# Kernel tuning notes

Hardware: AMD Instinct MI355X
Metric: run time of the kernel (lower is better)

The kernel has to match this reference:

```python
import jax, jax.numpy as jnp
import numpy as np

V, C = 100000, 400000          # variables, clauses
IN, OUT, H = 96, 64, 4         # in_channels, out_channels, heads
E_HALF = 1000000               # edges per direction
NEG_SLOPE = 0.2
LN_EPS = 1e-5


def _w(k, shape, fan_in):
    return (jax.random.normal(k, shape, jnp.float32) / np.sqrt(fan_in)).astype(jnp.float32)


def setup_inputs() -> dict:
    key = jax.random.key(0)
    ks = jax.random.split(key, 30)
    x = jax.random.normal(ks[0], (V + C, IN), jnp.float32)
    node_type = jnp.concatenate([jnp.full((V,), 1.0, jnp.float32), jnp.full((C,), 2.0, jnp.float32)])
    x = x.at[:, 0].set(node_type)  # NODE_TYPE_VAR=1, NODE_TYPE_CLAUSE=2
    # first half: "v2c" edges (source id >= num_vars), second half: "c2v" edges
    src1 = jax.random.randint(ks[1], (E_HALF,), V, 2 * V)   # -V -> index into x_var
    dst1 = jax.random.randint(ks[2], (E_HALF,), 0, C)       # index into x_clause
    src2 = jax.random.randint(ks[3], (E_HALF,), 0, V)       # index into h_c_new (V<=C so valid)
    dst2 = jax.random.randint(ks[4], (E_HALF,), V, 2 * V)   # -V -> index into x_var
    edge_index = jnp.stack([jnp.concatenate([src1, src2]),
                            jnp.concatenate([dst1, dst2])]).astype(jnp.int32)
    HD = H * OUT
    return {
        "x": x, "edge_index": edge_index, "num_vars": V,
        # v2c GATv2Conv (src=vars IN, dst=clauses IN)
        "v2c_Wl": _w(ks[5], (IN, HD), IN), "v2c_Wr": _w(ks[6], (IN, HD), IN),
        "v2c_att": _w(ks[7], (H, OUT), OUT), "v2c_bias": jnp.zeros((HD,), jnp.float32),
        "c_ln_g": jnp.ones((HD,), jnp.float32), "c_ln_b": jnp.zeros((HD,), jnp.float32),
        "c_Wih": _w(ks[8], (3 * OUT, HD), HD), "c_Whh": _w(ks[9], (3 * OUT, OUT), OUT),
        "c_bih": jnp.zeros((3 * OUT,), jnp.float32), "c_bhh": jnp.zeros((3 * OUT,), jnp.float32),
        # c2v GATv2Conv (src=clauses OUT, dst=vars IN)
        "c2v_Wl": _w(ks[10], (OUT, HD), OUT), "c2v_Wr": _w(ks[11], (IN, HD), IN),
        "c2v_att": _w(ks[12], (H, OUT), OUT), "c2v_bias": jnp.zeros((HD,), jnp.float32),
        "v_ln_g": jnp.ones((HD,), jnp.float32), "v_ln_b": jnp.zeros((HD,), jnp.float32),
        "v_Wih": _w(ks[13], (3 * OUT, HD), HD), "v_Whh": _w(ks[14], (3 * OUT, OUT), OUT),
        "v_bih": jnp.zeros((3 * OUT,), jnp.float32), "v_bhh": jnp.zeros((3 * OUT,), jnp.float32),
    }


def gatv2(x_src, x_dst, edge_index, Wl, Wr, att, bias, num_dst):
    """PyG GATv2Conv, concat=True, no self loops, eval mode (no attn dropout)."""
    h, d = att.shape
    xl = (x_src @ Wl).reshape(-1, h, d)   # [Ns, H, D]
    xr = (x_dst @ Wr).reshape(-1, h, d)   # [Nd, H, D]
    j, i = edge_index[0], edge_index[1]
    e = jax.nn.leaky_relu(xl[j] + xr[i], NEG_SLOPE)          # [E, H, D]
    alpha = jnp.einsum('ehd,hd->eh', e, att)                 # [E, H]
    amax = jax.ops.segment_max(alpha, i, num_segments=num_dst)
    alpha = jnp.exp(alpha - amax[i])
    denom = jax.ops.segment_sum(alpha, i, num_segments=num_dst)
    alpha = alpha / (denom[i] + 1e-16)
    msg = xl[j] * alpha[..., None]                           # [E, H, D]
    out = jax.ops.segment_sum(msg, i, num_segments=num_dst)  # [num_dst, H, D]
    return out.reshape(num_dst, h * d) + bias


def layernorm(x, g, b):
    mu = jnp.mean(x, axis=-1, keepdims=True)
    var = jnp.mean((x - mu) ** 2, axis=-1, keepdims=True)
    return (x - mu) * jax.lax.rsqrt(var + LN_EPS) * g + b


def gru_cell(x, hprev, Wih, Whh, bih, bhh):
    gi = x @ Wih.T + bih      # [N, 3*OUT]
    gh = hprev @ Whh.T + bhh  # [N, 3*OUT]
    ir, iz, inn = jnp.split(gi, 3, axis=-1)
    hr, hz, hn = jnp.split(gh, 3, axis=-1)
    r = jax.nn.sigmoid(ir + hr)
    z = jax.nn.sigmoid(iz + hz)
    n = jnp.tanh(inn + r * hn)
    return (1.0 - z) * n + z * hprev


def reference(x, edge_index, num_vars,
              v2c_Wl, v2c_Wr, v2c_att, v2c_bias, c_ln_g, c_ln_b,
              c_Wih, c_Whh, c_bih, c_bhh,
              c2v_Wl, c2v_Wr, c2v_att, c2v_bias, v_ln_g, v_ln_b,
              v_Wih, v_Whh, v_bih, v_bhh):
    out_ch = c_Whh.shape[1]
    n_nodes = x.shape[0]
    n_cla = n_nodes - num_vars
    h_old = x[:, -out_ch:]
    x_var, x_cla = x[:num_vars], x[num_vars:]           # vars first, clauses after
    h_v_old, h_c_old = h_old[:num_vars], h_old[num_vars:]
    e_half = edge_index.shape[1] // 2
    # edges with edge_index[0] >= num_vars (first half by construction), shift row 0
    v2c = jnp.stack([edge_index[0, :e_half] - num_vars, edge_index[1, :e_half]])
    m_c = gatv2(x_var, x_cla, v2c, v2c_Wl, v2c_Wr, v2c_att, v2c_bias, n_cla)
    m_c = layernorm(m_c, c_ln_g, c_ln_b)                # dropout = identity (eval)
    h_c_new = gru_cell(m_c, h_c_old, c_Wih, c_Whh, c_bih, c_bhh)
    # edges with edge_index[0] < num_vars (second half), shift row 1
    c2v = jnp.stack([edge_index[0, e_half:], edge_index[1, e_half:] - num_vars])
    m_v = gatv2(h_c_new, x_var, c2v, c2v_Wl, c2v_Wr, c2v_att, c2v_bias, num_vars)
    m_v = layernorm(m_v, v_ln_g, v_ln_b)
    h_v_new = gru_cell(m_v, h_v_old, v_Wih, v_Whh, v_bih, v_bhh)
    # x_new[var_mask]=h_v_new; x_new[clause_mask]=h_c_new (vars-first layout)
    return jnp.concatenate([h_v_new, h_c_new], axis=0)
```

## Files before the change

### kernel.cpp

```cpp
#include <hip/hip_runtime.h>
#include <hip/hip_bf16.h>
#include <cstdint>
#include <cstddef>

constexpr int V_NODES = 100000;
constexpr float NEG = 0.2f;
constexpr float LN_EPS = 1e-5f;
typedef __hip_bfloat16 bf16;

typedef __attribute__((ext_vector_type(8))) short short8v;
typedef __attribute__((ext_vector_type(4))) float f32x4;

__device__ inline float bflo(unsigned u){ return __uint_as_float(u << 16); }
__device__ inline float bfhi(unsigned u){ return __uint_as_float(u & 0xffff0000u); }
__device__ inline unsigned short f2bu(float x){ bf16 h = __float2bfloat16(x); return *reinterpret_cast<unsigned short*>(&h); }
__device__ inline unsigned bfpk(float x, float y){ return (unsigned)f2bu(x) | ((unsigned)f2bu(y) << 16); }

__device__ inline f32x4 mfma16(short8v a, short8v b, f32x4 c){
  return __builtin_amdgcn_mfma_f32_16x16x32_bf16(a, b, c, 0, 0, 0);
}

__device__ inline float sigm_f(float v){ return __builtin_amdgcn_rcpf(1.f + __expf(-v)); }
__device__ inline float tanh_f(float t){ return 1.f - 2.f*__builtin_amdgcn_rcpf(__expf(2.f*t) + 1.f); }

__global__ __launch_bounds__(256) void wprep_gf(const float* __restrict__ W,
                                                bf16* __restrict__ Wf, int K){
  int tid = blockIdx.x*256 + threadIdx.x;
  if (tid >= K*256) return;
  int fi = tid >> 9, rem = tid & 511;
  int lane = rem >> 3, i = rem & 7;
  int ks = fi >> 4, nt = fi & 15;
  int n = nt*16 + (lane & 15);
  int k = ks*32 + ((lane >> 4) << 3) + i;
  Wf[tid] = __float2bfloat16(W[(size_t)k*256 + n]);
}

__global__ __launch_bounds__(256) void wprep_gp(const float* __restrict__ W,
                                                bf16* __restrict__ Wf, int K){
  int tid = blockIdx.x*256 + threadIdx.x;
  if (tid >= K*256) return;
  int fi = tid >> 9, rem = tid & 511;
  int lane = rem >> 3, i = rem & 7;
  int ks = fi >> 4, nt = fi & 15;
  int n = nt*16 + (lane & 15);
  int ns = (((n & 63) >> 4) << 6) + ((n & 15) << 2) + (n >> 6);
  int k = ks*32 + ((lane >> 4) << 3) + i;
  Wf[tid] = __float2bfloat16(W[(size_t)k*256 + ns]);
}

__global__ __launch_bounds__(256) void wprep_bu(const float* __restrict__ Wih,
                                                const float* __restrict__ Whh,
                                                float* __restrict__ Bm){
  int tid = blockIdx.x*256 + threadIdx.x;
  if (tid >= 81920) return;
  int k = tid >> 8, n = tid & 255;
  float v = 0.f;
  if (k < 256) {
    if (n < 192) v = Wih[(size_t)n*256 + k];
  } else {
    int kh = k - 256;
    if (n < 128)       v = Whh[(size_t)n*64 + kh];
    else if (n >= 192) v = Whh[(size_t)(n - 64)*64 + kh];
  }
  Bm[tid] = v;
}

__global__ __launch_bounds__(256) void gemm_mf(
    const float* __restrict__ A, int lda, int K,
    const bf16* __restrict__ Wf, bf16* __restrict__ outp, int M)
{
  const int l  = threadIdx.x & 63;
  const int w  = threadIdx.x >> 6;
  const int jl = l & 15, kg = l >> 4;
  const int row0 = blockIdx.x*64 + w*16;
  __shared__ __align__(16) short As4[4][16*104];
  short* Aw = As4[w];

  const int K2 = K >> 1;
  const int tot = 16 * K2;
  for (int idx = l; idx < tot; idx += 64) {
    int r = idx / K2, c = idx - r*K2;
    int row = row0 + r;
    float2 a = (row < M) ? *(const float2*)(A + (size_t)row*lda + 2*c)
                         : make_float2(0.f, 0.f);
    *(unsigned*)(Aw + r*104 + 2*c) = bfpk(a.x, a.y);
  }
  asm volatile("" ::: "memory");

  f32x4 acc[16];
#pragma unroll
  for (int nt = 0; nt < 16; ++nt) acc[nt] = (f32x4){0.f,0.f,0.f,0.f};

  const short* Wb = (const short*)Wf + l*8;
  const short* Ab = Aw + jl*104 + kg*8;
  const int NKS = K >> 5;
  for (int ks = 0; ks < NKS; ++ks) {
    short8v a = *(const short8v*)(Ab + ks*32);
#pragma unroll
    for (int nt = 0; nt < 16; ++nt) {
      short8v b = *(const short8v*)(Wb + (size_t)(ks*16 + nt)*512);
      acc[nt] = mfma16(a, b, acc[nt]);
    }
  }

#pragma unroll
  for (int r = 0; r < 4; ++r) {
    int row = row0 + kg*4 + r;
    if (row < M) {
#pragma unroll
      for (int nt2 = 0; nt2 < 4; ++nt2) {
        uint2 o;
        o.x = bfpk(acc[nt2][r],   acc[nt2+4][r]);
        o.y = bfpk(acc[nt2+8][r], acc[nt2+12][r]);
        ((uint2*)outp)[(size_t)row * 64 + (nt2*16 + jl)] = o;
      }
    }
  }
}

__global__ __launch_bounds__(256) void hist_k(const int* __restrict__ dst, int doff,
                                              int* __restrict__ cnt, int E){
  int e = blockIdx.x*256 + threadIdx.x;
  if (e < E) atomicAdd(&cnt[dst[e]-doff], 1);
}
__global__ __launch_bounds__(256) void scanA(const int* __restrict__ cnt, int* __restrict__ part,
                                             int* __restrict__ bsum, int D){
  __shared__ int ts[256];
  int base = blockIdx.x*2048 + threadIdx.x*8;
  int v[8]; int s = 0;
#pragma unroll
  for (int i = 0; i < 8; ++i){ int idx = base+i; v[i] = (idx < D) ? cnt[idx] : 0; s += v[i]; }
  ts[threadIdx.x] = s; __syncthreads();
  for (int off = 1; off < 256; off <<= 1){
    int o = (threadIdx.x >= off) ? ts[threadIdx.x - off] : 0;
    __syncthreads();
    ts[threadIdx.x] += o;
    __syncthreads();
  }
  int run = ts[threadIdx.x] - s;
#pragma unroll
  for (int i = 0; i < 8; ++i){ int idx = base+i; if (idx < D) part[idx] = run; run += v[i]; }
  if (threadIdx.x == 255) bsum[blockIdx.x] = ts[255];
}
__global__ __launch_bounds__(256) void scanB(int* __restrict__ bsum, int nb){
  __shared__ int ts[256];
  int v = (threadIdx.x < nb) ? bsum[threadIdx.x] : 0;
  ts[threadIdx.x] = v; __syncthreads();
  for (int off = 1; off < 256; off <<= 1){
    int o = (threadIdx.x >= off) ? ts[threadIdx.x - off] : 0;
    __syncthreads();
    ts[threadIdx.x] += o;
    __syncthreads();
  }
  if (threadIdx.x < nb) bsum[threadIdx.x] = ts[threadIdx.x] - v;
}
__global__ __launch_bounds__(256) void scanC(const int* __restrict__ part, const int* __restrict__ bsum,
                                             int* __restrict__ rowptr, int* __restrict__ cursor,
                                             int D, int E){
  int idx = blockIdx.x*256 + threadIdx.x;
  if (idx < D){ int v = part[idx] + bsum[idx >> 11]; rowptr[idx] = v; cursor[idx] = v; }
  if (idx == 0) rowptr[D] = E;
}
__global__ __launch_bounds__(256) void scatter_k(const int* __restrict__ src, int soff,
                                                 const int* __restrict__ dst, int doff,
                                                 int* __restrict__ cursor, int* __restrict__ col, int E){
  int e = blockIdx.x*256 + threadIdx.x;
  if (e >= E) return;
  int p = atomicAdd(&cursor[dst[e]-doff], 1);
  col[p] = src[e] - soff;
}

__global__ __launch_bounds__(256) void gat_agg(
    const int* __restrict__ rowptr, const int* __restrict__ col,
    const bf16* __restrict__ xl, const bf16* __restrict__ xr,
    const float* __restrict__ att,
    bf16* __restrict__ agg, int D)
{
  __shared__ short Tr4[4][256];
  int wid = (int)((blockIdx.x*256u + threadIdx.x) >> 6);
  if (wid >= D) return;
  const int l = threadIdx.x & 63;
  const int g = l >> 4, r = l & 15;
  short* Tw = Tr4[(threadIdx.x >> 6)];
  uint2 ur = ((const uint2*)xr)[(size_t)wid*64 + l];
  const float xr0 = bflo(ur.x), xr1 = bfhi(ur.x), xr2 = bflo(ur.y), xr3 = bfhi(ur.y);
  const float4 at = *(const float4*)(att + g*64 + 4*r);
  float lsum = 0.f;
  float a0=0.f, a1=0.f, a2=0.f, a3=0.f;
  int p0 = rowptr[wid], p1 = rowptr[wid+1];
  int p = p0;
  for (; p + 1 < p1; p += 2){
    int ja = col[p], jb = col[p+1];
    uint2 ua = ((const uint2*)xl)[(size_t)ja*64 + l];
    uint2 ub = ((const uint2*)xl)[(size_t)jb*64 + l];
    float xa0 = bflo(ua.x), xa1 = bfhi(ua.x), xa2 = bflo(ua.y), xa3 = bfhi(ua.y);
    float xb0 = bflo(ub.x), xb1 = bfhi(ub.x), xb2 = bflo(ub.y), xb3 = bfhi(ub.y);
    float ta0 = xa0+xr0; ta0 = (ta0 > 0.f ? ta0 : NEG*ta0);
    float ta1 = xa1+xr1; ta1 = (ta1 > 0.f ? ta1 : NEG*ta1);
    float ta2 = xa2+xr2; ta2 = (ta2 > 0.f ? ta2 : NEG*ta2);
    float ta3 = xa3+xr3; ta3 = (ta3 > 0.f ? ta3 : NEG*ta3);
    float tb0 = xb0+xr0; tb0 = (tb0 > 0.f ? tb0 : NEG*tb0);
    float tb1 = xb1+xr1; tb1 = (tb1 > 0.f ? tb1 : NEG*tb1);
    float tb2 = xb2+xr2; tb2 = (tb2 > 0.f ? tb2 : NEG*tb2);
    float tb3 = xb3+xr3; tb3 = (tb3 > 0.f ? tb3 : NEG*tb3);
    float sa = ta0*at.x + ta1*at.y + ta2*at.z + ta3*at.w;
    float sb = tb0*at.x + tb1*at.y + tb2*at.z + tb3*at.w;
    sa += __shfl_xor(sa, 8, 64);  sb += __shfl_xor(sb, 8, 64);
    sa += __shfl_xor(sa, 4, 64);  sb += __shfl_xor(sb, 4, 64);
    sa += __shfl_xor(sa, 2, 64);  sb += __shfl_xor(sb, 2, 64);
    sa += __shfl_xor(sa, 1, 64);  sb += __shfl_xor(sb, 1, 64);
    float pea = __expf(sa), peb = __expf(sb);
    lsum += pea + peb;
    a0 += pea*xa0 + peb*xb0;
    a1 += pea*xa1 + peb*xb1;
    a2 += pea*xa2 + peb*xb2;
    a3 += pea*xa3 + peb*xb3;
  }
  if (p < p1){
    int j = col[p];
    uint2 uj = ((const uint2*)xl)[(size_t)j*64 + l];
    float x0 = bflo(uj.x), x1 = bfhi(uj.x), x2 = bflo(uj.y), x3 = bfhi(uj.y);
    float t0 = x0+xr0; t0 = (t0 > 0.f ? t0 : NEG*t0);
    float t1 = x1+xr1; t1 = (t1 > 0.f ? t1 : NEG*t1);
    float t2 = x2+xr2; t2 = (t2 > 0.f ? t2 : NEG*t2);
    float t3 = x3+xr3; t3 = (t3 > 0.f ? t3 : NEG*t3);
    float s = t0*at.x + t1*at.y + t2*at.z + t3*at.w;
    s += __shfl_xor(s, 8, 64);
    s += __shfl_xor(s, 4, 64);
    s += __shfl_xor(s, 2, 64);
    s += __shfl_xor(s, 1, 64);
    float pe = __expf(s);
    lsum += pe;
    a0 += pe*x0; a1 += pe*x1; a2 += pe*x2; a3 += pe*x3;
  }
  float inv = 1.f/(lsum + 1e-16f);
  Tw[16*r +  0 + g] = (short)f2bu(a0*inv);
  Tw[16*r +  4 + g] = (short)f2bu(a1*inv);
  Tw[16*r +  8 + g] = (short)f2bu(a2*inv);
  Tw[16*r + 12 + g] = (short)f2bu(a3*inv);
  asm volatile("" ::: "memory");
  ((uint2*)agg)[(size_t)wid*64 + l] = ((const uint2*)Tw)[l];
}

__global__ __launch_bounds__(256) void ln_gemm(
    const bf16* __restrict__ agg,
    const float* __restrict__ gbias,
    const float* __restrict__ g, const float* __restrict__ b,
    const bf16* __restrict__ Wf,
    const float* __restrict__ bih, const float* __restrict__ bhh,
    const float* __restrict__ x, int hrow0,
    float* __restrict__ out, int orow0, int M)
{
  __shared__ __align__(16) short At[64*328];
  const int l  = threadIdx.x & 63;
  const int w  = threadIdx.x >> 6;
  const int row0 = blockIdx.x*64;
  const int jl = l & 15, kg = l >> 4;

  float gb0 = gbias[l], gb1 = gbias[64+l], gb2 = gbias[128+l], gb3 = gbias[192+l];
  float gg0 = g[l],     gg1 = g[64+l],    gg2 = g[128+l],    gg3 = g[192+l];
  float bt0 = b[l],     bt1 = b[64+l],    bt2 = b[128+l],    bt3 = b[192+l];
  uint2 av[16]; float hp[16];
#pragma unroll
  for (int rr = 0; rr < 16; ++rr) {
    int row = row0 + w*16 + rr;
    av[rr] = make_uint2(0u, 0u);
    hp[rr] = 0.f;
    if (row < M) {
      av[rr] = ((const uint2*)agg)[(size_t)row*64 + l];
      hp[rr] = x[(size_t)(hrow0+row)*96 + 32 + l];
    }
  }
#pragma unroll
  for (int rr = 0; rr < 16; ++rr) {
    int rloc = w*16 + rr;
    float f0 = bflo(av[rr].x) + gb0, f1 = bfhi(av[rr].x) + gb1;
    float f2 = bflo(av[rr].y) + gb2, f3 = bfhi(av[rr].y) + gb3;
    float s = f0+f1+f2+f3, ss = f0*f0+f1*f1+f2*f2+f3*f3;
#pragma unroll
    for (int off = 32; off; off >>= 1){ s += __shfl_xor(s,off,64); ss += __shfl_xor(ss,off,64); }
    float mean = s * (1.f/256.f);
    float var  = ss * (1.f/256.f) - mean*mean;
    float rstd = rsqrtf(var + LN_EPS);
    short* Ar = At + rloc*328;
    Ar[l]       = (short)f2bu((f0-mean)*rstd*gg0 + bt0);
    Ar[64 + l]  = (short)f2bu((f1-mean)*rstd*gg1 + bt1);
    Ar[128 + l] = (short)f2bu((f2-mean)*rstd*gg2 + bt2);
    Ar[192 + l] = (short)f2bu((f3-mean)*rstd*gg3 + bt3);
    Ar[256 + l] = (short)f2bu(hp[rr]);
  }
  __syncthreads();

  f32x4 acc[4][4];
#pragma unroll
  for (int mt = 0; mt < 4; ++mt)
#pragma unroll
    for (int q = 0; q < 4; ++q) acc[mt][q] = (f32x4){0.f,0.f,0.f,0.f};

  const short8v* Wl = (const short8v*)Wf + l;
  const short* Ab = At + jl*328 + kg*8;

  short8v cb0 = Wl[(0*16 + w)*64];
  short8v cb1 = Wl[(0*16 + 4 + w)*64];
  short8v cb2 = Wl[(0*16 + 8 + w)*64];
#pragma unroll
  for (int ks = 0; ks < 10; ++ks) {
    short8v nb0 = cb0, nb1 = cb1, nb2 = cb2;
    if (ks < 9) {
      const int kn = ks + 1;
      nb0 = Wl[(kn*16 + w)*64];
      nb1 = Wl[(kn*16 + 4 + w)*64];
      nb2 = Wl[(kn*16 + ((kn < 8) ? 8 : 12) + w)*64];
    }
    const int gi = (ks < 8) ? 2 : 3;
#pragma unroll
    for (int mt = 0; mt < 4; ++mt) {
      short8v a = *(const short8v*)(Ab + mt*16*328 + ks*32);
      acc[mt][0]  = mfma16(a, cb0, acc[mt][0]);
      acc[mt][1]  = mfma16(a, cb1, acc[mt][1]);
      acc[mt][gi] = mfma16(a, cb2, acc[mt][gi]);
    }
    cb0 = nb0; cb1 = nb1; cb2 = nb2;
  }

  const int j = 16*w + jl;
  const float br = bih[j]      + bhh[j];
  const float bz = bih[64+j]   + bhh[64+j];
  const float bn = bih[128+j];
  const float bh = bhh[128+j];
  float hv[16];
#pragma unroll
  for (int mt = 0; mt < 4; ++mt)
#pragma unroll
    for (int r = 0; r < 4; ++r) {
      int row = row0 + mt*16 + kg*4 + r;
      hv[mt*4+r] = (row < M) ? x[(size_t)(hrow0+row)*96 + 32 + j] : 0.f;
    }
#pragma unroll
  for (int mt = 0; mt < 4; ++mt) {
#pragma unroll
    for (int r = 0; r < 4; ++r) {
      int row = row0 + mt*16 + kg*4 + r;
      if (row < M) {
        float rg = sigm_f(acc[mt][0][r] + br);
        float zg = sigm_f(acc[mt][1][r] + bz);
        float ng = tanh_f(acc[mt][2][r] + bn + rg*(acc[mt][3][r] + bh));
        out[(size_t)(orow0+row)*64 + j] = (1.f - zg)*ng + zg*hv[mt*4+r];
      }
    }
  }
}

__global__ void sentinel_kernel(float* out){ out[0] = 123456.0f; }

extern "C" void kernel_launch(void* const* d_in, const int* in_sizes, int n_in,
                              void* d_out, int out_size, void* d_ws, size_t ws_size,
                              hipStream_t stream)
{
  const float* x        = (const float*)d_in[0];
  const int*   ei       = (const int*)d_in[1];
  const float* v2c_Wl   = (const float*)d_in[3];
  const float* v2c_Wr   = (const float*)d_in[4];
  const float* v2c_att  = (const float*)d_in[5];
  const float* v2c_bias = (const float*)d_in[6];
  const float* c_ln_g   = (const float*)d_in[7];
  const float* c_ln_b   = (const float*)d_in[8];
  const float* c_Wih    = (const float*)d_in[9];
  const float* c_Whh    = (const float*)d_in[10];
  const float* c_bih    = (const float*)d_in[11];
  const float* c_bhh    = (const float*)d_in[12];
  const float* c2v_Wl   = (const float*)d_in[13];
  const float* c2v_Wr   = (const float*)d_in[14];
  const float* c2v_att  = (const float*)d_in[15];
  const float* c2v_bias = (const float*)d_in[16];
  const float* v_ln_g   = (const float*)d_in[17];
  const float* v_ln_b   = (const float*)d_in[18];
  const float* v_Wih    = (const float*)d_in[19];
  const float* v_Whh    = (const float*)d_in[20];
  const float* v_bih    = (const float*)d_in[21];
  const float* v_bhh    = (const float*)d_in[22];
  float* out = (float*)d_out;

  const int V = V_NODES;
  const int C = in_sizes[0] / 96 - V;
  const int E = in_sizes[1] / 4;
  const int* e0_1 = ei;
  const int* e1_1 = ei + (size_t)2*E;
  const int* e0_2 = ei + (size_t)E;
  const int* e1_2 = ei + (size_t)3*E;

  bf16* xl  = (bf16*)d_ws;
  bf16* xr  = xl + (size_t)C*256;
  bf16* agg = xr + (size_t)C*256;
  bf16* Wf2 = agg + (size_t)C*256;
  float* Bm = (float*)(Wf2 + 81920);
  bf16* Wgf = (bf16*)(Bm + 81920);
  int* cnt    = (int*)(Wgf + 24576);
  int* rowptr = cnt + C;
  int* part   = rowptr + C + 1;
  int* bsum   = part + C;
  int* col    = bsum + 256;
  size_t need = (size_t)C*256*2*3 + (size_t)81920*2 + (size_t)81920*4 +
                (size_t)24576*2 + ((size_t)3*C + 1 + 256 + (size_t)E) * 4;
  if (ws_size < need) {
    hipMemsetAsync(d_out, 0, (size_t)out_size*4, stream);
    sentinel_kernel<<<1,1,0,stream>>>(out);
    return;
  }

  const int EB = (E + 255)/256;

  wprep_gp<<<96, 256, 0, stream>>>(v2c_Wl, Wgf, 96);
  gemm_mf<<<(V+63)/64, 256, 0, stream>>>(x, 96, 96, Wgf, xl, V);
  wprep_gp<<<96, 256, 0, stream>>>(v2c_Wr, Wgf, 96);
  gemm_mf<<<(C+63)/64, 256, 0, stream>>>(x + (size_t)V*96, 96, 96, Wgf, xr, C);
  hipMemsetAsync(cnt, 0, (size_t)C*4, stream);
  hist_k<<<EB, 256, 0, stream>>>(e1_1, 0, cnt, E);
  {
    int nb = (C + 2047)/2048;
    scanA<<<nb, 256, 0, stream>>>(cnt, part, bsum, C);
    scanB<<<1, 256, 0, stream>>>(bsum, nb);
    scanC<<<(C+255)/256, 256, 0, stream>>>(part, bsum, rowptr, cnt, C, E);
  }
  scatter_k<<<EB, 256, 0, stream>>>(e0_1, V, e1_1, 0, cnt, col, E);
  gat_agg<<<(C+3)/4, 256, 0, stream>>>(rowptr, col, xl, xr, v2c_att, agg, C);
  wprep_bu<<<320, 256, 0, stream>>>(c_Wih, c_Whh, Bm);
  wprep_gf<<<320, 256, 0, stream>>>(Bm, Wf2, 320);
  ln_gemm<<<(C+63)/64, 256, 0, stream>>>(agg, v2c_bias, c_ln_g, c_ln_b, Wf2,
                                         c_bih, c_bhh, x, V, out, V, C);

  wprep_gp<<<64, 256, 0, stream>>>(c2v_Wl, Wgf, 64);
  gemm_mf<<<(C+63)/64, 256, 0, stream>>>(out + (size_t)V*64, 64, 64, Wgf, xl, C);
  wprep_gp<<<96, 256, 0, stream>>>(c2v_Wr, Wgf, 96);
  gemm_mf<<<(V+63)/64, 256, 0, stream>>>(x, 96, 96, Wgf, xr, V);
  hipMemsetAsync(cnt, 0, (size_t)V*4, stream);
  hist_k<<<EB, 256, 0, stream>>>(e1_2, V, cnt, E);
  {
    int nb = (V + 2047)/2048;
    scanA<<<nb, 256, 0, stream>>>(cnt, part, bsum, V);
    scanB<<<1, 256, 0, stream>>>(bsum, nb);
    scanC<<<(V+255)/256, 256, 0, stream>>>(part, bsum, rowptr, cnt, V, E);
  }
  scatter_k<<<EB, 256, 0, stream>>>(e0_2, 0, e1_2, V, cnt, col, E);
  gat_agg<<<(V+3)/4, 256, 0, stream>>>(rowptr, col, xl, xr, c2v_att, agg, V);
  wprep_bu<<<320, 256, 0, stream>>>(v_Wih, v_Whh, Bm);
  wprep_gf<<<320, 256, 0, stream>>>(Bm, Wf2, 320);
  ln_gemm<<<(V+63)/64, 256, 0, stream>>>(agg, c2v_bias, v_ln_g, v_ln_b, Wf2,
                                         v_bih, v_bhh, x, 0, out, 0, V);
}
```

Baseline: 1.108 ms.

## Split GEMM N-dimension across waves and share A tile in LDS with B prefetch

The MFMA projection GEMM now stages a shared 64-row bf16 A tile in LDS for the whole block. Each wave computes all 64 rows but only a quarter of the N tiles, instead of 16 rows across all N tiles. The aim is to cut redundant global/L2 loads of the weight fragments, which each wave previously read in full, and to register-prefetch the next k-step's B fragments to hide load latency. In exchange it adds a block-wide barrier, and the column interleaving used on output must still line up with the packed weight layout.

Result: faster. 1.045 ms (-5.7%).

```diff
diff --git a/kernel.cpp b/kernel.cpp
--- a/kernel.cpp
+++ b/kernel.cpp
@@ -72,47 +72,63 @@
   const int l  = threadIdx.x & 63;
   const int w  = threadIdx.x >> 6;
   const int jl = l & 15, kg = l >> 4;
-  const int row0 = blockIdx.x*64 + w*16;
-  __shared__ __align__(16) short As4[4][16*104];
-  short* Aw = As4[w];
+  const int row0 = blockIdx.x*64;
+  __shared__ __align__(16) short As[64*104];
 
   const int K2 = K >> 1;
-  const int tot = 16 * K2;
-  for (int idx = l; idx < tot; idx += 64) {
+  const int tot = 64 * K2;
+  for (int idx = threadIdx.x; idx < tot; idx += 256) {
     int r = idx / K2, c = idx - r*K2;
     int row = row0 + r;
     float2 a = (row < M) ? *(const float2*)(A + (size_t)row*lda + 2*c)
                          : make_float2(0.f, 0.f);
-    *(unsigned*)(Aw + r*104 + 2*c) = bfpk(a.x, a.y);
-  }
-  asm volatile("" ::: "memory");
-
-  f32x4 acc[16];
-#pragma unroll
-  for (int nt = 0; nt < 16; ++nt) acc[nt] = (f32x4){0.f,0.f,0.f,0.f};
-
-  const short* Wb = (const short*)Wf + l*8;
-  const short* Ab = Aw + jl*104 + kg*8;
+    *(unsigned*)(As + r*104 + 2*c) = bfpk(a.x, a.y);
+  }
+  __syncthreads();
+
+  f32x4 acc[4][4];
+#pragma unroll
+  for (int mt = 0; mt < 4; ++mt)
+#pragma unroll
+    for (int q = 0; q < 4; ++q) acc[mt][q] = (f32x4){0.f,0.f,0.f,0.f};
+
+  const short8v* Wl = (const short8v*)Wf + l;
+  const short* Ab = As + jl*104 + kg*8;
   const int NKS = K >> 5;
+
+  short8v cb[4];
+#pragma unroll
+  for (int q = 0; q < 4; ++q) cb[q] = Wl[(0*16 + 4*q + w)*64];
   for (int ks = 0; ks < NKS; ++ks) {
-    short8v a = *(const short8v*)(Ab + ks*32);
-#pragma unroll
-    for (int nt = 0; nt < 16; ++nt) {
-      short8v b = *(const short8v*)(Wb + (size_t)(ks*16 + nt)*512);
-      acc[nt] = mfma16(a, b, acc[nt]);
-    }
-  }
-
-#pragma unroll
-  for (int r = 0; r < 4; ++r) {
-    int row = row0 + kg*4 + r;
-    if (row < M) {
-#pragma unroll
-      for (int nt2 = 0; nt2 < 4; ++nt2) {
+    short8v nb[4];
+#pragma unroll
+    for (int q = 0; q < 4; ++q) nb[q] = cb[q];
+    if (ks + 1 < NKS) {
+#pragma unroll
+      for (int q = 0; q < 4; ++q) nb[q] = Wl[((ks+1)*16 + 4*q + w)*64];
+    }
+#pragma unroll
+    for (int mt = 0; mt < 4; ++mt) {
+      short8v a = *(const short8v*)(Ab + mt*16*104 + ks*32);
+      acc[mt][0] = mfma16(a, cb[0], acc[mt][0]);
+      acc[mt][1] = mfma16(a, cb[1], acc[mt][1]);
+      acc[mt][2] = mfma16(a, cb[2], acc[mt][2]);
+      acc[mt][3] = mfma16(a, cb[3], acc[mt][3]);
+    }
+#pragma unroll
+    for (int q = 0; q < 4; ++q) cb[q] = nb[q];
+  }
+
+#pragma unroll
+  for (int mt = 0; mt < 4; ++mt) {
+#pragma unroll
+    for (int r = 0; r < 4; ++r) {
+      int row = row0 + mt*16 + kg*4 + r;
+      if (row < M) {
         uint2 o;
-        o.x = bfpk(acc[nt2][r],   acc[nt2+4][r]);
-        o.y = bfpk(acc[nt2+8][r], acc[nt2+12][r]);
-        ((uint2*)outp)[(size_t)row * 64 + (nt2*16 + jl)] = o;
+        o.x = bfpk(acc[mt][0][r], acc[mt][1][r]);
+        o.y = bfpk(acc[mt][2][r], acc[mt][3][r]);
+        ((uint2*)outp)[(size_t)row*64 + (16*w + jl)] = o;
       }
     }
   }
```
